# Performance work log

Measured on AMD Instinct MI355X. Metric: run time of the kernel, lower is better.

The kernel has to match this reference:

```python
import jax, jax.numpy as jnp
import numpy as np

B, C, L, H, D = 2, 1024, 2048, 16, 64  # batch, n_factor, seq, heads, head_dim
LN_EPS = 1e-5


def setup_inputs() -> dict:
    key = jax.random.key(0)
    ks = jax.random.split(key, 8)
    s = 0.02
    return {
        "x": jax.random.normal(ks[0], (B, C, L), jnp.float32),
        "y": jax.random.normal(ks[1], (B, C, L), jnp.float32),
        "Wq": jax.random.normal(ks[2], (H, C, D), jnp.float32) * s,
        "Wk": jax.random.normal(ks[3], (H, C, D), jnp.float32) * s,
        "Wv": jax.random.normal(ks[4], (H, C, D), jnp.float32) * s,
        "bq": jax.random.normal(ks[5], (H, D), jnp.float32) * s,
        "bk": jax.random.normal(ks[6], (H, D), jnp.float32) * s,
        "bv": jax.random.normal(ks[7], (H, D), jnp.float32) * s,
        "gamma": jnp.ones((C,), jnp.float32),
        "beta": jnp.zeros((C,), jnp.float32),
    }


def reference(x, y, Wq, Wk, Wv, bq, bk, bv, gamma, beta):
    # Per-head Conv1d(kernel=1) == per-position linear; batch all heads at once.
    # x,y: [B, C, L]; W*: [H, C, D]; result q/k/v: [B, H, L, D]
    q = jnp.einsum('bcl,hcd->bhld', x, Wq) + bq[None, :, None, :]
    k = jnp.einsum('bcl,hcd->bhld', y, Wk) + bk[None, :, None, :]
    v = jnp.einsum('bcl,hcd->bhld', y, Wv) + bv[None, :, None, :]

    scale = 1.0 / jnp.sqrt(jnp.float32(D))  # n_factor_head ** 0.5
    scores = jnp.einsum('bhqd,bhkd->bhqk', q, k) * scale  # [B,H,L,L]
    attn = jax.nn.softmax(scores, axis=-1)
    ctx = jnp.einsum('bhqk,bhkd->bhqd', attn, v)  # [B,H,L,D]

    # torch.cat over heads along last dim == [B, L, H*D]
    att = jnp.transpose(ctx, (0, 2, 1, 3)).reshape(B, L, H * D)

    h = jnp.transpose(x, (0, 2, 1)) + att  # residual on x permuted to [B,L,C]
    mu = jnp.mean(h, axis=-1, keepdims=True)
    var = jnp.var(h, axis=-1, keepdims=True)
    out = (h - mu) * jax.lax.rsqrt(var + LN_EPS) * gamma + beta
    # dropout: identity in eval mode
    return out
```

## Files before the change

### kernel.cpp

```cpp
#include <hip/hip_runtime.h>
#include <hip/hip_bf16.h>

#define DEVI __device__ __forceinline__

typedef unsigned short u16;
typedef __bf16 bf16x8 __attribute__((ext_vector_type(8)));
typedef float f32x4 __attribute__((ext_vector_type(4)));

constexpr int Bn = 2, Cn = 1024, Ln = 2048, Hn = 16, Dn = 64;

DEVI u16 f2bfu(float f) { return __builtin_bit_cast(u16, __float2bfloat16(f)); }
DEVI float bfu2f(u16 u) { return __bfloat162float(__builtin_bit_cast(__hip_bfloat16, u)); }
DEVI f32x4 mfma16(bf16x8 a, bf16x8 b, f32x4 c) {
  return __builtin_amdgcn_mfma_f32_16x16x32_bf16(a, b, c, 0, 0, 0);
}
DEVI unsigned pk2(float lo, float hi) {
  return (unsigned)f2bfu(lo) | ((unsigned)f2bfu(hi) << 16);
}
DEVI void gld16(const u16* g, u16* l) {
  __builtin_amdgcn_global_load_lds(
      (const __attribute__((address_space(1))) unsigned*)g,
      (__attribute__((address_space(3))) unsigned*)l, 16, 0, 0);
}
DEVI int fsw(int row) { return (row & 7) ^ (((row >> 3) & 1) << 2); }

__global__ __launch_bounds__(256) void transpose_xy(const float* __restrict__ x,
                                                    const float* __restrict__ y,
                                                    u16* __restrict__ xT,
                                                    u16* __restrict__ yT) {
  int z = blockIdx.z;
  int which = z >> 1, b = z & 1;
  const float* src = (which ? y : x) + (size_t)b * Cn * Ln;
  u16* dst = (which ? yT : xT) + (size_t)b * Ln * Cn;
  int l0 = blockIdx.x * 64, c0 = blockIdx.y * 64;
  __shared__ float tile[64][65];
  int t = threadIdx.x;
  #pragma unroll
  for (int i = 0; i < 16; ++i) {
    int idx = i * 256 + t;
    int r = idx >> 6, cc = idx & 63;
    tile[r][cc] = src[(size_t)(c0 + r) * Ln + (l0 + cc)];
  }
  __syncthreads();
  #pragma unroll
  for (int i = 0; i < 8; ++i) {
    int idx = i * 256 + t;
    int r = idx >> 5, cc = (idx & 31) * 2;
    unsigned pkv = pk2(tile[cc][r], tile[cc + 1][r]);
    *(unsigned*)(&dst[(size_t)(l0 + r) * Cn + (c0 + cc)]) = pkv;
  }
}

__global__ __launch_bounds__(256) void transpose_w(const float* __restrict__ Wq,
                                                   const float* __restrict__ Wk,
                                                   const float* __restrict__ Wv,
                                                   u16* __restrict__ WT) {
  int c0 = blockIdx.x * 64, h = blockIdx.y, which = blockIdx.z;
  const float* src = (which == 0 ? Wq : (which == 1 ? Wk : Wv)) + (size_t)h * Cn * Dn;
  u16* dst = WT + ((size_t)which * Hn + h) * Dn * Cn;
  __shared__ float tile[64][65];
  int t = threadIdx.x;
  #pragma unroll
  for (int i = 0; i < 16; ++i) {
    int idx = i * 256 + t;
    int r = idx >> 6, cc = idx & 63;
    tile[r][cc] = src[(size_t)(c0 + r) * Dn + cc];
  }
  __syncthreads();
  #pragma unroll
  for (int i = 0; i < 16; ++i) {
    int idx = i * 256 + t;
    int r = idx >> 6, cc = idx & 63;
    dst[(size_t)r * Cn + (c0 + cc)] = f2bfu(tile[cc][r]);
  }
}

__global__ __launch_bounds__(256) void gemm_qkv3(const u16* __restrict__ xT,
                                                 const u16* __restrict__ yT,
                                                 const u16* __restrict__ WT,
                                                 const float* __restrict__ bq,
                                                 const float* __restrict__ bk,
                                                 const float* __restrict__ bv,
                                                 u16* __restrict__ Qb,
                                                 u16* __restrict__ Kb,
                                                 u16* __restrict__ Vt) {
  int mt = blockIdx.x, by = blockIdx.y, b = blockIdx.z;
  int which = by >> 3, hp = by & 7;
  const u16* A = (which == 0 ? xT : yT) + (size_t)b * Ln * Cn + (size_t)mt * 128 * Cn;
  const u16* Bw = WT + ((size_t)which * 1024 + (size_t)hp * 128) * Cn;
  __shared__ __align__(16) u16 smem[2 * 128 * 64];
  u16* lA = smem;
  u16* lB = smem + 128 * 64;
  int t = threadIdx.x, wave = t >> 6, lane = t & 63;
  int wr = wave >> 1, wc = wave & 1;
  int ml = lane & 15, kg = lane >> 4;
  f32x4 acc[4][4] = {};
  for (int k0 = 0; k0 < Cn; k0 += 64) {
    __syncthreads();
    #pragma unroll
    for (int j = 0; j < 4; ++j) {
      int q = wave * 256 + j * 64 + lane;
      int row = q >> 3, p = q & 7, c16 = p ^ (row & 7);
      gld16(A + (size_t)row * Cn + k0 + c16 * 8, &lA[(wave * 256 + j * 64) * 8]);
    }
    #pragma unroll
    for (int j = 0; j < 4; ++j) {
      int q = wave * 256 + j * 64 + lane;
      int row = q >> 3, p = q & 7, c16 = p ^ (row & 7);
      gld16(Bw + (size_t)row * Cn + k0 + c16 * 8, &lB[(wave * 256 + j * 64) * 8]);
    }
    __syncthreads();
    bf16x8 af[4][2], bf[4][2];
    #pragma unroll
    for (int m = 0; m < 4; ++m) {
      int row = wr * 64 + m * 16 + ml;
      #pragma unroll
      for (int kk = 0; kk < 2; ++kk) {
        int p = (kk * 4 + kg) ^ (row & 7);
        af[m][kk] = *(const bf16x8*)(&lA[row * 64 + p * 8]);
      }
    }
    #pragma unroll
    for (int n = 0; n < 4; ++n) {
      int row = wc * 64 + n * 16 + ml;
      #pragma unroll
      for (int kk = 0; kk < 2; ++kk) {
        int p = (kk * 4 + kg) ^ (row & 7);
        bf[n][kk] = *(const bf16x8*)(&lB[row * 64 + p * 8]);
      }
    }
    __builtin_amdgcn_s_setprio(1);
    #pragma unroll
    for (int m = 0; m < 4; ++m)
      #pragma unroll
      for (int n = 0; n < 4; ++n)
        #pragma unroll
        for (int kk = 0; kk < 2; ++kk)
          acc[m][n] = mfma16(af[m][kk], bf[n][kk], acc[m][n]);
    __builtin_amdgcn_s_setprio(0);
  }
  int head = hp * 2 + wc;
  const float* bp = (which == 0 ? bq : (which == 1 ? bk : bv));
  if (which < 2) {
    u16* O = (which == 0 ? Qb : Kb) + (((size_t)b * Hn + head) * Ln + (size_t)mt * 128) * Dn;
    #pragma unroll
    for (int n = 0; n < 4; ++n) {
      float bvv = bp[head * 64 + n * 16 + ml];
      #pragma unroll
      for (int m = 0; m < 4; ++m)
        #pragma unroll
        for (int r = 0; r < 4; ++r) {
          int row = wr * 64 + m * 16 + kg * 4 + r;
          O[(size_t)row * Dn + n * 16 + ml] = f2bfu(acc[m][n][r] + bvv);
        }
    }
  } else {
    __syncthreads();
    #pragma unroll
    for (int n = 0; n < 4; ++n) {
      float bvv = bp[head * 64 + n * 16 + ml];
      int n_loc = wc * 64 + n * 16 + ml;
      int swz = (n_loc & 7) << 4;
      #pragma unroll
      for (int m = 0; m < 4; ++m) {
        int m_base = wr * 64 + m * 16 + kg * 4;
        uint2 pkd;
        pkd.x = pk2(acc[m][n][0] + bvv, acc[m][n][1] + bvv);
        pkd.y = pk2(acc[m][n][2] + bvv, acc[m][n][3] + bvv);
        *(uint2*)(&smem[n_loc * 128 + (m_base ^ swz)]) = pkd;
      }
    }
    __syncthreads();
    u16* Vbase = Vt + ((size_t)b * Hn + hp * 2) * Dn * Ln + (size_t)mt * 128;
    #pragma unroll
    for (int i = 0; i < 8; ++i) {
      int chunk = i * 256 + t;
      int n = chunk >> 4, cc = chunk & 15;
      uint4 vv = *(const uint4*)(&smem[n * 128 + (cc ^ ((n & 7) << 1)) * 8]);
      *(uint4*)(Vbase + (size_t)n * Ln + cc * 8) = vv;
    }
  }
}

__global__ __launch_bounds__(512, 8) void flash_attn(const u16* __restrict__ Qg,
                                                     const u16* __restrict__ Kg,
                                                     const u16* __restrict__ Vtg,
                                                     u16* __restrict__ att) {
  int n = blockIdx.x + 32 * (blockIdx.y + 16 * blockIdx.z);
  int xcd = n & 7, m = n >> 3;
  int grp = xcd * 4 + (m >> 5);
  int qt = m & 31;
  int h = grp & 15, b = grp >> 4;

  size_t bh = (size_t)b * Hn + h;
  const u16* Qp = Qg + (bh * Ln + (size_t)qt * 64) * Dn;
  const u16* Kp = Kg + bh * Ln * Dn;
  const u16* Vp = Vtg + bh * Dn * Ln;
  int t = threadIdx.x, wave = t >> 6, lane = t & 63;
  int qs = wave & 3, g = wave >> 2;
  int ml = lane & 15, kg = lane >> 4;
  __shared__ __align__(16) u16 Kl[2][64 * 64];
  __shared__ __align__(16) u16 Vl[2][64 * 64];

  constexpr float QS = 0.125f * 1.44269504f;
  bf16x8 qf[2];
  #pragma unroll
  for (int kk = 0; kk < 2; ++kk) {
    bf16x8 raw = *(const bf16x8*)(Qp + (size_t)(qs * 16 + ml) * Dn + kk * 32 + kg * 8);
    #pragma unroll
    for (int j = 0; j < 8; ++j) raw[j] = (__bf16)((float)raw[j] * QS);
    qf[kk] = raw;
  }

  f32x4 ctx[4] = {};
  float psum = 0.f;

  int koff[2][2], voff[4];
  {
    #pragma unroll
    for (int nt = 0; nt < 2; ++nt) {
      int rowk = g * 32 + 8 * (ml >> 2) + 4 * nt + (ml & 3);
      #pragma unroll
      for (int kk = 0; kk < 2; ++kk)
        koff[nt][kk] = rowk * 64 + (((kk * 4 + kg) ^ fsw(rowk)) << 3);
    }
    #pragma unroll
    for (int nt = 0; nt < 4; ++nt) {
      int rowv = nt * 16 + ml;
      voff[nt] = rowv * 64 + ((((g * 4 + kg) ^ fsw(rowv))) << 3);
    }
  }
  int rowk_st = t >> 3;
  int c16_st = ((t & 7) ^ fsw(rowk_st)) * 8;

  auto stage = [&](int buf, int kv0) {
    gld16(Kp + (size_t)(kv0 + rowk_st) * Dn + c16_st, &Kl[buf][wave * 512]);
    gld16(Vp + (size_t)rowk_st * Ln + kv0 + c16_st, &Vl[buf][wave * 512]);
  };

  constexpr int NT = Ln / 64;

  auto tile = [&](int cur, int tt) {
    if (tt + 1 < NT) {
      stage(cur ^ 1, (tt + 1) * 64);
      asm volatile("s_waitcnt vmcnt(2)" ::: "memory");
    } else {
      asm volatile("s_waitcnt vmcnt(0)" ::: "memory");
    }
    __builtin_amdgcn_s_barrier();
    __builtin_amdgcn_sched_barrier(0);
    const u16* Kh = Kl[cur];
    const u16* Vh = Vl[cur];
    f32x4 s[2] = {};
    __builtin_amdgcn_s_setprio(1);
    #pragma unroll
    for (int nt = 0; nt < 2; ++nt)
      #pragma unroll
      for (int kk = 0; kk < 2; ++kk) {
        bf16x8 kf = *(const bf16x8*)(&Kh[koff[nt][kk]]);
        s[nt] = mfma16(kf, qf[kk], s[nt]);
      }
    __builtin_amdgcn_s_setprio(0);
    f32x4 e0, e1;
    #pragma unroll
    for (int r = 0; r < 4; ++r) e0[r] = __builtin_amdgcn_exp2f(s[0][r]);
    #pragma unroll
    for (int r = 0; r < 4; ++r) e1[r] = __builtin_amdgcn_exp2f(s[1][r]);
    psum += (e0[0] + e0[1]) + (e0[2] + e0[3]) + (e1[0] + e1[1]) + (e1[2] + e1[3]);
    uint4 pw;
    pw.x = pk2(e0[0], e0[1]);
    pw.y = pk2(e0[2], e0[3]);
    pw.z = pk2(e1[0], e1[1]);
    pw.w = pk2(e1[2], e1[3]);
    bf16x8 pf = __builtin_bit_cast(bf16x8, pw);
    __builtin_amdgcn_s_setprio(1);
    #pragma unroll
    for (int nt = 0; nt < 4; ++nt) {
      bf16x8 vf = *(const bf16x8*)(&Vh[voff[nt]]);
      ctx[nt] = mfma16(pf, vf, ctx[nt]);
    }
    __builtin_amdgcn_s_setprio(0);
    asm volatile("s_waitcnt lgkmcnt(0)" ::: "memory");
    __builtin_amdgcn_s_barrier();
  };

  stage(0, 0);
  asm volatile("s_waitcnt vmcnt(0)" ::: "memory");
  __builtin_amdgcn_s_barrier();

  for (int tt = 0; tt < NT; tt += 2) {
    tile(0, tt);
    tile(1, tt + 1);
  }

  __syncthreads();
  float* comb = (float*)&Kl[0][0];
  float* psA = (float*)&Vl[0][0];
  if (g == 1) {
    int base = qs * 1024 + lane;
    #pragma unroll
    for (int nt = 0; nt < 4; ++nt)
      #pragma unroll
      for (int r = 0; r < 4; ++r)
        comb[base + (nt * 4 + r) * 64] = ctx[nt][r];
    psA[qs * 64 + lane] = psum;
  }
  __syncthreads();
  if (g == 0) {
    int base = qs * 1024 + lane;
    #pragma unroll
    for (int nt = 0; nt < 4; ++nt)
      #pragma unroll
      for (int r = 0; r < 4; ++r)
        ctx[nt][r] += comb[base + (nt * 4 + r) * 64];
    psum += psA[qs * 64 + lane];
    psum += __shfl_xor(psum, 16);
    psum += __shfl_xor(psum, 32);
    float inv[4];
    #pragma unroll
    for (int r = 0; r < 4; ++r) inv[r] = 1.f / __shfl(psum, kg * 4 + r);
    #pragma unroll
    for (int nt = 0; nt < 4; ++nt)
      #pragma unroll
      for (int r = 0; r < 4; ++r) {
        size_t row = (size_t)b * Ln + qt * 64 + qs * 16 + kg * 4 + r;
        att[row * Cn + h * Dn + nt * 16 + ml] = f2bfu(ctx[nt][r] * inv[r]);
      }
  }
}

__global__ __launch_bounds__(256) void ln_kernel(const u16* __restrict__ att,
                                                 const u16* __restrict__ xT,
                                                 const float* __restrict__ gamma,
                                                 const float* __restrict__ beta,
                                                 float* __restrict__ out) {
  size_t row = blockIdx.x;
  const u16* ap = att + row * Cn;
  const u16* xp = xT + row * Cn;
  float* op = out + row * Cn;
  int t = threadIdx.x;
  ushort4 a4 = *(const ushort4*)(ap + t * 4);
  ushort4 xv = *(const ushort4*)(xp + t * 4);
  float h0 = bfu2f(a4.x) + bfu2f(xv.x), h1 = bfu2f(a4.y) + bfu2f(xv.y);
  float h2 = bfu2f(a4.z) + bfu2f(xv.z), h3 = bfu2f(a4.w) + bfu2f(xv.w);
  float s = h0 + h1 + h2 + h3;
  float ss = h0 * h0 + h1 * h1 + h2 * h2 + h3 * h3;
  #pragma unroll
  for (int off = 1; off < 64; off <<= 1) {
    s += __shfl_xor(s, off);
    ss += __shfl_xor(ss, off);
  }
  __shared__ float red[8];
  int wave = t >> 6, lane = t & 63;
  if (lane == 0) { red[wave] = s; red[wave + 4] = ss; }
  __syncthreads();
  s = red[0] + red[1] + red[2] + red[3];
  ss = red[4] + red[5] + red[6] + red[7];
  float mu = s * (1.f / 1024.f);
  float var = ss * (1.f / 1024.f) - mu * mu;
  float rinv = rsqrtf(var + 1e-5f);
  float4 gmv = *(const float4*)(gamma + t * 4);
  float4 bev = *(const float4*)(beta + t * 4);
  float4 o;
  o.x = (h0 - mu) * rinv * gmv.x + bev.x;
  o.y = (h1 - mu) * rinv * gmv.y + bev.y;
  o.z = (h2 - mu) * rinv * gmv.z + bev.z;
  o.w = (h3 - mu) * rinv * gmv.w + bev.w;
  *(float4*)(op + t * 4) = o;
}

extern "C" void kernel_launch(void* const* d_in, const int* in_sizes, int n_in,
                              void* d_out, int out_size, void* d_ws, size_t ws_size,
                              hipStream_t stream) {
  const float* x = (const float*)d_in[0];
  const float* y = (const float*)d_in[1];
  const float* Wq = (const float*)d_in[2];
  const float* Wk = (const float*)d_in[3];
  const float* Wv = (const float*)d_in[4];
  const float* bq = (const float*)d_in[5];
  const float* bk = (const float*)d_in[6];
  const float* bv = (const float*)d_in[7];
  const float* gamma = (const float*)d_in[8];
  const float* beta = (const float*)d_in[9];
  float* out = (float*)d_out;

  char* ws = (char*)d_ws;
  u16* xT = (u16*)(ws + 0);
  u16* yT = (u16*)(ws + 8388608);
  u16* WT = (u16*)(ws + 16777216);
  u16* Qb = (u16*)(ws + 23068672);
  u16* Kb = (u16*)(ws + 31457280);
  u16* VT = (u16*)(ws + 39845888);
  u16* att = (u16*)(ws + 48234496);

  transpose_xy<<<dim3(Ln / 64, Cn / 64, 4), dim3(256), 0, stream>>>(x, y, xT, yT);
  transpose_w<<<dim3(Cn / 64, Hn, 3), dim3(256), 0, stream>>>(Wq, Wk, Wv, WT);
  gemm_qkv3<<<dim3(Ln / 128, 24, Bn), dim3(256), 0, stream>>>(xT, yT, WT, bq, bk, bv, Qb, Kb, VT);
  flash_attn<<<dim3(Ln / 64, Hn, Bn), dim3(512), 0, stream>>>(Qb, Kb, VT, att);
  ln_kernel<<<dim3(Bn * Ln), dim3(256), 0, stream>>>(att, xT, gamma, beta, out);
}
```

Baseline: 108.5 us.

## Halve attention block to 4 waves, each wave handling two query subtiles

New measurement: 106.5 us. Within noise of the previous version (-1.9%).

```diff
diff --git a/kernel.cpp b/kernel.cpp
--- a/kernel.cpp
+++ b/kernel.cpp
@@ -182,7 +182,7 @@
   }
 }
 
-__global__ __launch_bounds__(512, 8) void flash_attn(const u16* __restrict__ Qg,
+__global__ __launch_bounds__(256, 4) void flash_attn(const u16* __restrict__ Qg,
                                                      const u16* __restrict__ Kg,
                                                      const u16* __restrict__ Vtg,
                                                      u16* __restrict__ att) {
@@ -197,23 +197,25 @@
   const u16* Kp = Kg + bh * Ln * Dn;
   const u16* Vp = Vtg + bh * Dn * Ln;
   int t = threadIdx.x, wave = t >> 6, lane = t & 63;
-  int qs = wave & 3, g = wave >> 2;
+  int qs = wave & 1, g = wave >> 1;
   int ml = lane & 15, kg = lane >> 4;
   __shared__ __align__(16) u16 Kl[2][64 * 64];
   __shared__ __align__(16) u16 Vl[2][64 * 64];
 
   constexpr float QS = 0.125f * 1.44269504f;
-  bf16x8 qf[2];
-  #pragma unroll
-  for (int kk = 0; kk < 2; ++kk) {
-    bf16x8 raw = *(const bf16x8*)(Qp + (size_t)(qs * 16 + ml) * Dn + kk * 32 + kg * 8);
-    #pragma unroll
-    for (int j = 0; j < 8; ++j) raw[j] = (__bf16)((float)raw[j] * QS);
-    qf[kk] = raw;
-  }
-
-  f32x4 ctx[4] = {};
-  float psum = 0.f;
+  bf16x8 qf[2][2];
+  #pragma unroll
+  for (int qg = 0; qg < 2; ++qg)
+    #pragma unroll
+    for (int kk = 0; kk < 2; ++kk) {
+      bf16x8 raw = *(const bf16x8*)(Qp + (size_t)(qs * 32 + qg * 16 + ml) * Dn + kk * 32 + kg * 8);
+      #pragma unroll
+      for (int j = 0; j < 8; ++j) raw[j] = (__bf16)((float)raw[j] * QS);
+      qf[qg][kk] = raw;
+    }
+
+  f32x4 ctx[2][4] = {};
+  float psum[2] = {0.f, 0.f};
 
   int koff[2][2], voff[4];
   {
@@ -230,12 +232,23 @@
       voff[nt] = rowv * 64 + ((((g * 4 + kg) ^ fsw(rowv))) << 3);
     }
   }
-  int rowk_st = t >> 3;
-  int c16_st = ((t & 7) ^ fsw(rowk_st)) * 8;
+  int row_st[2], c16_st[2];
+  #pragma unroll
+  for (int j = 0; j < 2; ++j) {
+    int q = j * 256 + t;
+    row_st[j] = q >> 3;
+    c16_st[j] = ((q & 7) ^ fsw(row_st[j])) * 8;
+  }
 
   auto stage = [&](int buf, int kv0) {
-    gld16(Kp + (size_t)(kv0 + rowk_st) * Dn + c16_st, &Kl[buf][wave * 512]);
-    gld16(Vp + (size_t)rowk_st * Ln + kv0 + c16_st, &Vl[buf][wave * 512]);
+    #pragma unroll
+    for (int j = 0; j < 2; ++j)
+      gld16(Kp + (size_t)(kv0 + row_st[j]) * Dn + c16_st[j],
+            &Kl[buf][(j * 256 + wave * 64) * 8]);
+    #pragma unroll
+    for (int j = 0; j < 2; ++j)
+      gld16(Vp + (size_t)row_st[j] * Ln + kv0 + c16_st[j],
+            &Vl[buf][(j * 256 + wave * 64) * 8]);
   };
 
   constexpr int NT = Ln / 64;
@@ -243,7 +256,7 @@
   auto tile = [&](int cur, int tt) {
     if (tt + 1 < NT) {
       stage(cur ^ 1, (tt + 1) * 64);
-      asm volatile("s_waitcnt vmcnt(2)" ::: "memory");
+      asm volatile("s_waitcnt vmcnt(4)" ::: "memory");
     } else {
       asm volatile("s_waitcnt vmcnt(0)" ::: "memory");
     }
@@ -251,33 +264,45 @@
     __builtin_amdgcn_sched_barrier(0);
     const u16* Kh = Kl[cur];
     const u16* Vh = Vl[cur];
-    f32x4 s[2] = {};
+    bf16x8 kf[2][2];
+    #pragma unroll
+    for (int nt = 0; nt < 2; ++nt)
+      #pragma unroll
+      for (int kk = 0; kk < 2; ++kk)
+        kf[nt][kk] = *(const bf16x8*)(&Kh[koff[nt][kk]]);
+    f32x4 s[2][2] = {};
     __builtin_amdgcn_s_setprio(1);
     #pragma unroll
     for (int nt = 0; nt < 2; ++nt)
       #pragma unroll
-      for (int kk = 0; kk < 2; ++kk) {
-        bf16x8 kf = *(const bf16x8*)(&Kh[koff[nt][kk]]);
-        s[nt] = mfma16(kf, qf[kk], s[nt]);
-      }
+      for (int kk = 0; kk < 2; ++kk)
+        #pragma unroll
+        for (int qg = 0; qg < 2; ++qg)
+          s[qg][nt] = mfma16(kf[nt][kk], qf[qg][kk], s[qg][nt]);
     __builtin_amdgcn_s_setprio(0);
-    f32x4 e0, e1;
-    #pragma unroll
-    for (int r = 0; r < 4; ++r) e0[r] = __builtin_amdgcn_exp2f(s[0][r]);
-    #pragma unroll
-    for (int r = 0; r < 4; ++r) e1[r] = __builtin_amdgcn_exp2f(s[1][r]);
-    psum += (e0[0] + e0[1]) + (e0[2] + e0[3]) + (e1[0] + e1[1]) + (e1[2] + e1[3]);
-    uint4 pw;
-    pw.x = pk2(e0[0], e0[1]);
-    pw.y = pk2(e0[2], e0[3]);
-    pw.z = pk2(e1[0], e1[1]);
-    pw.w = pk2(e1[2], e1[3]);
-    bf16x8 pf = __builtin_bit_cast(bf16x8, pw);
+    bf16x8 pf[2];
+    #pragma unroll
+    for (int qg = 0; qg < 2; ++qg) {
+      f32x4 e0, e1;
+      #pragma unroll
+      for (int r = 0; r < 4; ++r) e0[r] = __builtin_amdgcn_exp2f(s[qg][0][r]);
+      #pragma unroll
+      for (int r = 0; r < 4; ++r) e1[r] = __builtin_amdgcn_exp2f(s[qg][1][r]);
+      psum[qg] += (e0[0] + e0[1]) + (e0[2] + e0[3]) + (e1[0] + e1[1]) + (e1[2] + e1[3]);
+      uint4 pw;
+      pw.x = pk2(e0[0], e0[1]);
+      pw.y = pk2(e0[2], e0[3]);
+      pw.z = pk2(e1[0], e1[1]);
+      pw.w = pk2(e1[2], e1[3]);
+      pf[qg] = __builtin_bit_cast(bf16x8, pw);
+    }
     __builtin_amdgcn_s_setprio(1);
     #pragma unroll
     for (int nt = 0; nt < 4; ++nt) {
       bf16x8 vf = *(const bf16x8*)(&Vh[voff[nt]]);
-      ctx[nt] = mfma16(pf, vf, ctx[nt]);
+      #pragma unroll
+      for (int qg = 0; qg < 2; ++qg)
+        ctx[qg][nt] = mfma16(pf[qg], vf, ctx[qg][nt]);
     }
     __builtin_amdgcn_s_setprio(0);
     asm volatile("s_waitcnt lgkmcnt(0)" ::: "memory");
@@ -297,35 +322,42 @@
   float* comb = (float*)&Kl[0][0];
   float* psA = (float*)&Vl[0][0];
   if (g == 1) {
-    int base = qs * 1024 + lane;
-    #pragma unroll
-    for (int nt = 0; nt < 4; ++nt)
-      #pragma unroll
-      for (int r = 0; r < 4; ++r)
-        comb[base + (nt * 4 + r) * 64] = ctx[nt][r];
-    psA[qs * 64 + lane] = psum;
+    #pragma unroll
+    for (int qg = 0; qg < 2; ++qg) {
+      #pragma unroll
+      for (int nt = 0; nt < 4; ++nt)
+        #pragma unroll
+        for (int r = 0; r < 4; ++r)
+          comb[(((qs * 2 + qg) * 16) + nt * 4 + r) * 64 + lane] = ctx[qg][nt][r];
+      psA[(qs * 2 + qg) * 64 + lane] = psum[qg];
+    }
   }
   __syncthreads();
   if (g == 0) {
-    int base = qs * 1024 + lane;
-    #pragma unroll
-    for (int nt = 0; nt < 4; ++nt)
-      #pragma unroll
-      for (int r = 0; r < 4; ++r)
-        ctx[nt][r] += comb[base + (nt * 4 + r) * 64];
-    psum += psA[qs * 64 + lane];
-    psum += __shfl_xor(psum, 16);
-    psum += __shfl_xor(psum, 32);
-    float inv[4];
-    #pragma unroll
-    for (int r = 0; r < 4; ++r) inv[r] = 1.f / __shfl(psum, kg * 4 + r);
-    #pragma unroll
-    for (int nt = 0; nt < 4; ++nt)
-      #pragma unroll
-      for (int r = 0; r < 4; ++r) {
-        size_t row = (size_t)b * Ln + qt * 64 + qs * 16 + kg * 4 + r;
-        att[row * Cn + h * Dn + nt * 16 + ml] = f2bfu(ctx[nt][r] * inv[r]);
-      }
+    #pragma unroll
+    for (int qg = 0; qg < 2; ++qg) {
+      #pragma unroll
+      for (int nt = 0; nt < 4; ++nt)
+        #pragma unroll
+        for (int r = 0; r < 4; ++r)
+          ctx[qg][nt][r] += comb[(((qs * 2 + qg) * 16) + nt * 4 + r) * 64 + lane];
+      psum[qg] += psA[(qs * 2 + qg) * 64 + lane];
+      psum[qg] += __shfl_xor(psum[qg], 16);
+      psum[qg] += __shfl_xor(psum[qg], 32);
+    }
+    #pragma unroll
+    for (int qg = 0; qg < 2; ++qg) {
+      float inv[4];
+      #pragma unroll
+      for (int r = 0; r < 4; ++r) inv[r] = 1.f / __shfl(psum[qg], kg * 4 + r);
+      #pragma unroll
+      for (int nt = 0; nt < 4; ++nt)
+        #pragma unroll
+        for (int r = 0; r < 4; ++r) {
+          size_t row = (size_t)b * Ln + qt * 64 + qs * 32 + qg * 16 + kg * 4 + r;
+          att[row * Cn + h * Dn + nt * 16 + ml] = f2bfu(ctx[qg][nt][r] * inv[r]);
+        }
+    }
   }
 }
 
@@ -396,6 +428,6 @@
   transpose_xy<<<dim3(Ln / 64, Cn / 64, 4), dim3(256), 0, stream>>>(x, y, xT, yT);
   transpose_w<<<dim3(Cn / 64, Hn, 3), dim3(256), 0, stream>>>(Wq, Wk, Wv, WT);
   gemm_qkv3<<<dim3(Ln / 128, 24, Bn), dim3(256), 0, stream>>>(xT, yT, WT, bq, bk, bv, Qb, Kb, VT);
-  flash_attn<<<dim3(Ln / 64, Hn, Bn), dim3(512), 0, stream>>>(Qb, Kb, VT, att);
+  flash_attn<<<dim3(Ln / 64, Hn, Bn), dim3(256), 0, stream>>>(Qb, Kb, VT, att);
   ln_kernel<<<dim3(Bn * Ln), dim3(256), 0, stream>>>(att, xT, gamma, beta, out);
 }
```
